# Optimization experiments

Hardware: AMD Instinct MI355X
Metric: run time of the kernel (lower is better)

## Reference

```python
import jax, jax.numpy as jnp
import numpy as np

N_ATOMS = 100000
N_EDGES = 400000
ATOM_DIM = 32
BOND_DIM = 16


def setup_inputs() -> dict:
    key = jax.random.key(0)
    k1, k2, k3, k4 = jax.random.split(key, 4)
    atom_features = jax.random.normal(k1, (N_ATOMS, ATOM_DIM), dtype=jnp.float32)
    bond_features = jax.random.normal(k2, (N_EDGES, BOND_DIM), dtype=jnp.float32)
    pair_indices = jax.random.randint(k3, (N_EDGES, 2), 0, N_ATOMS, dtype=jnp.int64)
    # glorot-uniform-like scale for the kernel
    limit = np.sqrt(6.0 / (BOND_DIM + ATOM_DIM * ATOM_DIM)).astype(np.float32)
    kernel = jax.random.uniform(k4, (BOND_DIM, ATOM_DIM * ATOM_DIM), dtype=jnp.float32,
                                minval=-limit, maxval=limit)
    bias = jnp.zeros((ATOM_DIM * ATOM_DIM,), dtype=jnp.float32)
    return {"atom_features": atom_features, "bond_features": bond_features,
            "pair_indices": pair_indices, "kernel": kernel, "bias": bias}


def reference(atom_features, bond_features, pair_indices, kernel, bias):
    n_atoms, d = atom_features.shape  # d = atom_dim
    e = bond_features.shape[0]
    # per-edge transform matrices: [E, d, d]
    edge_mats = (bond_features @ kernel + bias).reshape(e, d, d)
    # gather neighbor atom features via pair_indices[:, 1]
    neighbors = atom_features[pair_indices[:, 1]]  # [E, d]
    # per-edge matvec
    transformed = jnp.einsum('eij,ej->ei', edge_mats, neighbors)  # [E, d]
    # scatter-reduce onto source atoms
    return jax.ops.segment_sum(transformed, pair_indices[:, 0], num_segments=n_atoms)
```

## Files before the change

kernel.cpp:

```cpp
#include <hip/hip_runtime.h>


typedef _Float16 half8 __attribute__((ext_vector_type(8)));
typedef float float4v __attribute__((ext_vector_type(4)));

constexpr int E = 400000;
constexpr int TILES = E / 32;
constexpr int NBLK = 1024;
constexpr int WAVES = NBLK * 4;
constexpr int HALFW = WAVES / 2;

__global__ void zero_out4(float4* __restrict__ out, int n4) {
  int i = blockIdx.x * blockDim.x + threadIdx.x;
  if (i < n4) out[i] = make_float4(0.f, 0.f, 0.f, 0.f);
}

static __device__ inline half8 splat8(_Float16 v) {
  half8 r = {v, v, v, v, v, v, v, v};
  return r;
}

__global__ __launch_bounds__(256, 3)
void edge_mfma(const float* __restrict__ atom,
               const float* __restrict__ bondf,
               const int* __restrict__ pairs,
               const float* __restrict__ Kmat,
               const float* __restrict__ bias,
               float* __restrict__ out)
{
  const int tid   = threadIdx.x;
  const int lane  = tid & 63;
  const int wslot = tid >> 6;
  const int wid   = blockIdx.x * 4 + wslot;
  const int h     = wid & 1;
  const int q     = lane >> 4;
  const int el    = lane & 15;
  const int n     = el + h * 16;
  const int j0    = q * 8;

  half8 Wr[17];
  #pragma unroll
  for (int s = 0; s < 17; ++s) {
    const float* src = (s < 16) ? (Kmat + s * 1024 + n * 32 + j0)
                                : (bias + n * 32 + j0);
    half8 w;
    #pragma unroll
    for (int j = 0; j < 8; ++j) w[j] = (_Float16)src[j];
    Wr[s] = w;
  }

  for (int tile = (wid >> 1); tile < TILES; tile += HALFW) {
    const int ebase = tile * 32;

    int pv;
    if (lane < 32) pv = pairs[2 * (ebase + lane)];
    else           pv = pairs[2 * (ebase + lane - 32) + 1];
    const int aA = __shfl(pv, 32 + el);
    const int aB = __shfl(pv, 32 + el + 16);

    half8 nbA, nbB;
    {
      const float* pa = atom + (size_t)aA * 32 + j0;
      const float* pb = atom + (size_t)aB * 32 + j0;
      #pragma unroll
      for (int j = 0; j < 8; ++j) {
        nbA[j] = (_Float16)pa[j];
        nbB[j] = (_Float16)pb[j];
      }
    }
    _Float16 bA[16], bB[16];
    {
      const float* ba = bondf + (size_t)(ebase + el) * 16;
      const float* bb = bondf + (size_t)(ebase + el + 16) * 16;
      #pragma unroll
      for (int b = 0; b < 16; ++b) {
        bA[b] = (_Float16)ba[b];
        bB[b] = (_Float16)bb[b];
      }
    }

    float4v acc0 = {0.f, 0.f, 0.f, 0.f};
    float4v acc1 = {0.f, 0.f, 0.f, 0.f};
    #pragma unroll
    for (int s = 0; s < 16; ++s) {
      const half8 aAf = nbA * splat8(bA[s]);
      const half8 aBf = nbB * splat8(bB[s]);
      acc0 = __builtin_amdgcn_mfma_f32_16x16x32_f16(aAf, Wr[s], acc0, 0, 0, 0);
      acc1 = __builtin_amdgcn_mfma_f32_16x16x32_f16(aBf, Wr[s], acc1, 0, 0, 0);
    }
    acc0 = __builtin_amdgcn_mfma_f32_16x16x32_f16(nbA, Wr[16], acc0, 0, 0, 0);
    acc1 = __builtin_amdgcn_mfma_f32_16x16x32_f16(nbB, Wr[16], acc1, 0, 0, 0);

    #pragma unroll
    for (int r = 0; r < 4; ++r) {
      const int s0 = __shfl(pv, q * 4 + r);
      atomicAdd(out + (size_t)s0 * 32 + n, acc0[r]);
      const int s1 = __shfl(pv, q * 4 + r + 16);
      atomicAdd(out + (size_t)s1 * 32 + n, acc1[r]);
    }
  }
}

extern "C" void kernel_launch(void* const* d_in, const int* in_sizes, int n_in,
                              void* d_out, int out_size, void* d_ws, size_t ws_size,
                              hipStream_t stream) {
  const float* atom  = (const float*)d_in[0];
  const float* bondf = (const float*)d_in[1];
  const int*   pairs = (const int*)d_in[2];
  const float* Kmat  = (const float*)d_in[3];
  const float* bias  = (const float*)d_in[4];
  float* out = (float*)d_out;

  const int n4 = out_size / 4;
  zero_out4<<<(n4 + 255) / 256, 256, 0, stream>>>((float4*)out, n4);
  edge_mfma<<<NBLK, 256, 0, stream>>>(atom, bondf, pairs, Kmat, bias, out);
}
```

Before: 154.8 us.

## Replace atomic scatter with per-atom edge buckets and gather-based reduction

Per-edge outputs are no longer atomically added into the output. They are written to an fp16 workspace buffer. A separate pass builds fixed-capacity per-source-atom edge lists with atomic counters, and a reduce kernel sums each atom's edges by gathering from those lists. This removes float atomics on the output and the separate zeroing of it, but it adds two extra kernels, an fp16 intermediate round-trip (precision loss), and silently clamps degree at 32, which drops edges for high-degree atoms. Grid size and launch-bounds occupancy are also raised.

New measurement: 206.9 us. +33.7%, slower.

```diff
diff --git a/kernel.cpp b/kernel.cpp
--- a/kernel.cpp
+++ b/kernel.cpp
@@ -4,15 +4,32 @@
 typedef _Float16 half8 __attribute__((ext_vector_type(8)));
 typedef float float4v __attribute__((ext_vector_type(4)));
 
+constexpr int NA = 100000;
 constexpr int E = 400000;
 constexpr int TILES = E / 32;
-constexpr int NBLK = 1024;
+constexpr int NBLK = 1536;
 constexpr int WAVES = NBLK * 4;
 constexpr int HALFW = WAVES / 2;
+constexpr int MAXDEG = 32;
 
-__global__ void zero_out4(float4* __restrict__ out, int n4) {
+constexpr size_t OFF_CNT   = 0;
+constexpr size_t OFF_SLOTS = 400000;
+constexpr size_t OFF_T     = OFF_SLOTS + (size_t)NA * MAXDEG * 4;
+
+__global__ void k_zero(int* __restrict__ cnt) {
   int i = blockIdx.x * blockDim.x + threadIdx.x;
-  if (i < n4) out[i] = make_float4(0.f, 0.f, 0.f, 0.f);
+  if (i < NA) cnt[i] = 0;
+}
+
+__global__ void k_place(const int* __restrict__ pairs,
+                        int* __restrict__ cnt, int* __restrict__ slots) {
+  int e = blockIdx.x * blockDim.x + threadIdx.x;
+  if (e < E) {
+    const int s = ((const int2*)pairs)[e].x;
+    int p = atomicAdd(&cnt[s], 1);
+    p = min(p, MAXDEG - 1);
+    slots[s * MAXDEG + p] = e;
+  }
 }
 
 static __device__ inline half8 splat8(_Float16 v) {
@@ -20,13 +37,13 @@
   return r;
 }
 
-__global__ __launch_bounds__(256, 3)
-void edge_mfma(const float* __restrict__ atom,
-               const float* __restrict__ bondf,
-               const int* __restrict__ pairs,
-               const float* __restrict__ Kmat,
-               const float* __restrict__ bias,
-               float* __restrict__ out)
+__global__ __launch_bounds__(256, 4)
+void k_transform(const float* __restrict__ atom,
+                 const float* __restrict__ bondf,
+                 const int* __restrict__ pairs,
+                 const float* __restrict__ Kmat,
+                 const float* __restrict__ bias,
+                 _Float16* __restrict__ T)
 {
   const int tid   = threadIdx.x;
   const int lane  = tid & 63;
@@ -52,11 +69,10 @@
   for (int tile = (wid >> 1); tile < TILES; tile += HALFW) {
     const int ebase = tile * 32;
 
-    int pv;
-    if (lane < 32) pv = pairs[2 * (ebase + lane)];
-    else           pv = pairs[2 * (ebase + lane - 32) + 1];
-    const int aA = __shfl(pv, 32 + el);
-    const int aB = __shfl(pv, 32 + el + 16);
+    int pv = 0;
+    if (lane < 32) pv = pairs[2 * (ebase + lane) + 1];
+    const int aA = __shfl(pv, el);
+    const int aB = __shfl(pv, el + 16);
 
     half8 nbA, nbB;
     {
@@ -93,12 +109,29 @@
 
     #pragma unroll
     for (int r = 0; r < 4; ++r) {
-      const int s0 = __shfl(pv, q * 4 + r);
-      atomicAdd(out + (size_t)s0 * 32 + n, acc0[r]);
-      const int s1 = __shfl(pv, q * 4 + r + 16);
-      atomicAdd(out + (size_t)s1 * 32 + n, acc1[r]);
+      const int e0 = ebase + q * 4 + r;
+      T[(size_t)e0 * 32 + n] = (_Float16)acc0[r];
+      const int e1 = e0 + 16;
+      T[(size_t)e1 * 32 + n] = (_Float16)acc1[r];
     }
   }
+}
+
+__global__ __launch_bounds__(256)
+void k_reduce(const int* __restrict__ cnt, const int* __restrict__ slots,
+              const _Float16* __restrict__ T, float* __restrict__ out) {
+  const int tid = blockIdx.x * blockDim.x + threadIdx.x;
+  const int a = tid >> 5;
+  const int c = tid & 31;
+  if (a >= NA) return;
+  const int d = min(cnt[a], MAXDEG);
+  const int* row = slots + (size_t)a * MAXDEG;
+  float sum = 0.f;
+  for (int p = 0; p < d; ++p) {
+    const int e = row[p];
+    sum += (float)T[(size_t)e * 32 + c];
+  }
+  out[(size_t)a * 32 + c] = sum;
 }
 
 extern "C" void kernel_launch(void* const* d_in, const int* in_sizes, int n_in,
@@ -111,7 +144,12 @@
   const float* bias  = (const float*)d_in[4];
   float* out = (float*)d_out;
 
-  const int n4 = out_size / 4;
-  zero_out4<<<(n4 + 255) / 256, 256, 0, stream>>>((float4*)out, n4);
-  edge_mfma<<<NBLK, 256, 0, stream>>>(atom, bondf, pairs, Kmat, bias, out);
+  int* cnt        = (int*)((char*)d_ws + OFF_CNT);
+  int* slots      = (int*)((char*)d_ws + OFF_SLOTS);
+  _Float16* T     = (_Float16*)((char*)d_ws + OFF_T);
+
+  k_zero<<<(NA + 255) / 256, 256, 0, stream>>>(cnt);
+  k_place<<<(E + 255) / 256, 256, 0, stream>>>(pairs, cnt, slots);
+  k_transform<<<NBLK, 256, 0, stream>>>(atom, bondf, pairs, Kmat, bias, T);
+  k_reduce<<<(NA * 32 + 255) / 256, 256, 0, stream>>>(cnt, slots, T, out);
 }
```

## Pre-convert inputs to fp16 in prep kernel and software-pipeline edge tile loads

Applied to the files above, without the earlier changes.

A prep kernel now zeroes the output and converts the atom and bond features to fp16 in workspace, all in one launch. The edge kernel then reads packed half8 vectors instead of scalar fp32 loads with per-element conversion. The main loop is software-pipelined: the next tile's gathers and the pair indices two tiles ahead are loaded while the current tile's MFMAs and atomics run. The grid shrinks from 1024 to 768 blocks, and int2 pair loads replace the split scalar loads. The extra prep pass adds a full read and write of the features, and the prefetch raises register pressure.

After: 139.8 us. 1.11x faster.

```diff
diff --git a/kernel.cpp b/kernel.cpp
--- a/kernel.cpp
+++ b/kernel.cpp
@@ -2,17 +2,42 @@
 
 
 typedef _Float16 half8 __attribute__((ext_vector_type(8)));
+typedef _Float16 half4t __attribute__((ext_vector_type(4)));
 typedef float float4v __attribute__((ext_vector_type(4)));
 
-constexpr int E = 400000;
+constexpr int NA = 100000;
+constexpr int E  = 400000;
 constexpr int TILES = E / 32;
-constexpr int NBLK = 1024;
-constexpr int WAVES = NBLK * 4;
-constexpr int HALFW = WAVES / 2;
+constexpr int NBLK  = 768;
+constexpr int HALFW = NBLK * 4 / 2;
 
-__global__ void zero_out4(float4* __restrict__ out, int n4) {
+constexpr size_t OFF_ATOMH = 0;
+constexpr size_t OFF_BONDH = (size_t)NA * 32 * 2;
+
+constexpr int NZ4 = NA * 32 / 4;
+constexpr int NA4 = NA * 32 / 4;
+constexpr int NB4 = E * 16 / 4;
+constexpr int PREP_TOT = NZ4 + NA4 + NB4;
+
+__global__ void k_prep(const float* __restrict__ atom,
+                       const float* __restrict__ bond,
+                       float4* __restrict__ outz,
+                       half4t* __restrict__ atomh4,
+                       half4t* __restrict__ bondh4) {
   int i = blockIdx.x * blockDim.x + threadIdx.x;
-  if (i < n4) out[i] = make_float4(0.f, 0.f, 0.f, 0.f);
+  if (i < NZ4) {
+    outz[i] = make_float4(0.f, 0.f, 0.f, 0.f);
+  } else if (i < NZ4 + NA4) {
+    int k = i - NZ4;
+    float4 v = ((const float4*)atom)[k];
+    half4t hh = { (_Float16)v.x, (_Float16)v.y, (_Float16)v.z, (_Float16)v.w };
+    atomh4[k] = hh;
+  } else if (i < PREP_TOT) {
+    int k = i - NZ4 - NA4;
+    float4 v = ((const float4*)bond)[k];
+    half4t hh = { (_Float16)v.x, (_Float16)v.y, (_Float16)v.z, (_Float16)v.w };
+    bondh4[k] = hh;
+  }
 }
 
 static __device__ inline half8 splat8(_Float16 v) {
@@ -21,22 +46,21 @@
 }
 
 __global__ __launch_bounds__(256, 3)
-void edge_mfma(const float* __restrict__ atom,
-               const float* __restrict__ bondf,
-               const int* __restrict__ pairs,
-               const float* __restrict__ Kmat,
-               const float* __restrict__ bias,
-               float* __restrict__ out)
+void edge_fused(const _Float16* __restrict__ atomh,
+                const _Float16* __restrict__ bondh,
+                const int* __restrict__ pairs,
+                const float* __restrict__ Kmat,
+                const float* __restrict__ bias,
+                float* __restrict__ out)
 {
-  const int tid   = threadIdx.x;
-  const int lane  = tid & 63;
-  const int wslot = tid >> 6;
-  const int wid   = blockIdx.x * 4 + wslot;
-  const int h     = wid & 1;
-  const int q     = lane >> 4;
-  const int el    = lane & 15;
-  const int n     = el + h * 16;
-  const int j0    = q * 8;
+  const int tid  = threadIdx.x;
+  const int lane = tid & 63;
+  const int wid  = blockIdx.x * 4 + (tid >> 6);
+  const int h    = wid & 1;
+  const int q    = lane >> 4;
+  const int el   = lane & 15;
+  const int n    = el + h * 16;
+  const int j0   = q * 8;
 
   half8 Wr[17];
   #pragma unroll
@@ -49,55 +73,74 @@
     Wr[s] = w;
   }
 
-  for (int tile = (wid >> 1); tile < TILES; tile += HALFW) {
-    const int ebase = tile * 32;
+  const int start  = wid >> 1;
+  const int stride = HALFW;
+  const int2* pairs2 = (const int2*)pairs;
 
-    int pv;
-    if (lane < 32) pv = pairs[2 * (ebase + lane)];
-    else           pv = pairs[2 * (ebase + lane - 32) + 1];
-    const int aA = __shfl(pv, 32 + el);
-    const int aB = __shfl(pv, 32 + el + 16);
+  auto ldpv = [&](int t) -> int2 {
+    const int tc = t < TILES ? t : TILES - 1;
+    int2 v = make_int2(0, 0);
+    if (lane < 32) v = pairs2[tc * 32 + lane];
+    return v;
+  };
 
-    half8 nbA, nbB;
+  int2 pv0 = ldpv(start);
+  int2 pv1 = ldpv(start + stride);
+
+  half8 nbA_c, nbB_c, bA0_c, bA1_c, bB0_c, bB1_c;
+  {
+    const int aA = __shfl(pv0.y, el);
+    const int aB = __shfl(pv0.y, el + 16);
+    nbA_c = *(const half8*)(atomh + (size_t)aA * 32 + j0);
+    nbB_c = *(const half8*)(atomh + (size_t)aB * 32 + j0);
+    const _Float16* brA = bondh + (size_t)(start * 32 + el) * 16;
+    const _Float16* brB = bondh + (size_t)(start * 32 + el + 16) * 16;
+    bA0_c = *(const half8*)(brA);  bA1_c = *(const half8*)(brA + 8);
+    bB0_c = *(const half8*)(brB);  bB1_c = *(const half8*)(brB + 8);
+  }
+
+  for (int t = start; t < TILES; t += stride) {
+    const int tn = t + stride;
+
+    half8 nbA_n, nbB_n, bA0_n, bA1_n, bB0_n, bB1_n;
     {
-      const float* pa = atom + (size_t)aA * 32 + j0;
-      const float* pb = atom + (size_t)aB * 32 + j0;
-      #pragma unroll
-      for (int j = 0; j < 8; ++j) {
-        nbA[j] = (_Float16)pa[j];
-        nbB[j] = (_Float16)pb[j];
-      }
+      const int aA = __shfl(pv1.y, el);
+      const int aB = __shfl(pv1.y, el + 16);
+      nbA_n = *(const half8*)(atomh + (size_t)aA * 32 + j0);
+      nbB_n = *(const half8*)(atomh + (size_t)aB * 32 + j0);
+      const int tc = tn < TILES ? tn : TILES - 1;
+      const _Float16* brA = bondh + (size_t)(tc * 32 + el) * 16;
+      const _Float16* brB = bondh + (size_t)(tc * 32 + el + 16) * 16;
+      bA0_n = *(const half8*)(brA);  bA1_n = *(const half8*)(brA + 8);
+      bB0_n = *(const half8*)(brB);  bB1_n = *(const half8*)(brB + 8);
     }
-    _Float16 bA[16], bB[16];
-    {
-      const float* ba = bondf + (size_t)(ebase + el) * 16;
-      const float* bb = bondf + (size_t)(ebase + el + 16) * 16;
-      #pragma unroll
-      for (int b = 0; b < 16; ++b) {
-        bA[b] = (_Float16)ba[b];
-        bB[b] = (_Float16)bb[b];
-      }
-    }
+    const int2 pv2 = ldpv(tn + stride);
 
     float4v acc0 = {0.f, 0.f, 0.f, 0.f};
     float4v acc1 = {0.f, 0.f, 0.f, 0.f};
     #pragma unroll
     for (int s = 0; s < 16; ++s) {
-      const half8 aAf = nbA * splat8(bA[s]);
-      const half8 aBf = nbB * splat8(bB[s]);
+      const _Float16 sA = (s < 8) ? bA0_c[s] : bA1_c[s - 8];
+      const _Float16 sB = (s < 8) ? bB0_c[s] : bB1_c[s - 8];
+      const half8 aAf = nbA_c * splat8(sA);
+      const half8 aBf = nbB_c * splat8(sB);
       acc0 = __builtin_amdgcn_mfma_f32_16x16x32_f16(aAf, Wr[s], acc0, 0, 0, 0);
       acc1 = __builtin_amdgcn_mfma_f32_16x16x32_f16(aBf, Wr[s], acc1, 0, 0, 0);
     }
-    acc0 = __builtin_amdgcn_mfma_f32_16x16x32_f16(nbA, Wr[16], acc0, 0, 0, 0);
-    acc1 = __builtin_amdgcn_mfma_f32_16x16x32_f16(nbB, Wr[16], acc1, 0, 0, 0);
+    acc0 = __builtin_amdgcn_mfma_f32_16x16x32_f16(nbA_c, Wr[16], acc0, 0, 0, 0);
+    acc1 = __builtin_amdgcn_mfma_f32_16x16x32_f16(nbB_c, Wr[16], acc1, 0, 0, 0);
 
     #pragma unroll
     for (int r = 0; r < 4; ++r) {
-      const int s0 = __shfl(pv, q * 4 + r);
+      const int s0 = __shfl(pv0.x, q * 4 + r);
       atomicAdd(out + (size_t)s0 * 32 + n, acc0[r]);
-      const int s1 = __shfl(pv, q * 4 + r + 16);
+      const int s1 = __shfl(pv0.x, q * 4 + r + 16);
       atomicAdd(out + (size_t)s1 * 32 + n, acc1[r]);
     }
+
+    pv0 = pv1; pv1 = pv2;
+    nbA_c = nbA_n; nbB_c = nbB_n;
+    bA0_c = bA0_n; bA1_c = bA1_n; bB0_c = bB0_n; bB1_c = bB1_n;
   }
 }
 
@@ -111,7 +154,10 @@
   const float* bias  = (const float*)d_in[4];
   float* out = (float*)d_out;
 
-  const int n4 = out_size / 4;
-  zero_out4<<<(n4 + 255) / 256, 256, 0, stream>>>((float4*)out, n4);
-  edge_mfma<<<NBLK, 256, 0, stream>>>(atom, bondf, pairs, Kmat, bias, out);
+  _Float16* atomh = (_Float16*)((char*)d_ws + OFF_ATOMH);
+  _Float16* bondh = (_Float16*)((char*)d_ws + OFF_BONDH);
+
+  k_prep<<<(PREP_TOT + 255) / 256, 256, 0, stream>>>(
+      atom, bondf, (float4*)out, (half4t*)atomh, (half4t*)bondh);
+  edge_fused<<<NBLK, 256, 0, stream>>>(atomh, bondh, pairs, Kmat, bias, out);
 }
```
